# Optimization experiments

Hardware: AMD Instinct MI355X
Metric: run time of the kernel (lower is better)

Reference implementation:

```python
import jax, jax.numpy as jnp
import numpy as np

N = 100000   # nodes
E = 1250000  # directed edges
F = 32       # node_features
H = 64       # hidden_channels
C = 10       # num_classes
NEG_SLOPE = 0.2  # GATConv default LeakyReLU slope


def _glorot(key, shape):
    fan_in = shape[0]
    return jax.random.normal(key, shape, jnp.float32) / np.sqrt(fan_in)


def setup_inputs() -> dict:
    k = jax.random.split(jax.random.key(0), 16)
    x = jax.random.normal(k[0], (N, F), jnp.float32)
    edge_index = jax.random.randint(k[1], (2, E), 0, N, dtype=jnp.int32)
    return {
        "x": x,
        "edge_index": edge_index,
        # GCNConv 1
        "W1": _glorot(k[2], (F, H)), "b1": jnp.zeros((H,), jnp.float32),
        # GATConv (heads=1)
        "W2": _glorot(k[3], (H, H)),
        "a_src": _glorot(k[4], (H,)), "a_dst": _glorot(k[5], (H,)),
        "b2": jnp.zeros((H,), jnp.float32),
        # GCNConv 3
        "W3": _glorot(k[6], (H, H)), "b3": jnp.zeros((H,), jnp.float32),
        # optimization head
        "Wopt": _glorot(k[7], (H, C)), "bopt": jnp.zeros((C,), jnp.float32),
        # bottleneck detector MLP
        "Wb1": _glorot(k[8], (H, 32)), "bb1": jnp.zeros((32,), jnp.float32),
        "Wb2": _glorot(k[9], (32, 1)), "bb2": jnp.zeros((1,), jnp.float32),
    }


def _gcn_conv(x, W, b, src, dst, n):
    # PyG GCNConv: self-loops already appended to src/dst by caller.
    h = x @ W  # [n, out]
    deg = jnp.zeros((n,), x.dtype).at[dst].add(1.0)
    dinv = jax.lax.rsqrt(jnp.maximum(deg, 1e-12))
    norm = dinv[src] * dinv[dst]  # [e]
    msg = h[src] * norm[:, None]  # gather + scale
    out = jnp.zeros_like(h).at[dst].add(msg)  # scatter-add
    return out + b


def _gat_conv(x, W, a_src, a_dst, b, src, dst, n):
    # PyG GATConv, heads=1: self-loops already appended.
    h = x @ W  # [n, out]
    alpha_s = h @ a_src  # [n]
    alpha_d = h @ a_dst  # [n]
    e = jax.nn.leaky_relu(alpha_s[src] + alpha_d[dst], NEG_SLOPE)  # [e]
    # softmax over incoming edges of each dst node
    emax = jax.ops.segment_max(e, dst, num_segments=n)
    p = jnp.exp(e - emax[dst])
    denom = jax.ops.segment_sum(p, dst, num_segments=n)
    alpha = p / denom[dst]
    out = jnp.zeros_like(h).at[dst].add(h[src] * alpha[:, None])
    return out + b


def reference(x, edge_index, W1, b1, W2, a_src, a_dst, b2, W3, b3,
              Wopt, bopt, Wb1, bb1, Wb2, bb2):
    n = x.shape[0]
    loops = jnp.arange(n, dtype=edge_index.dtype)
    src = jnp.concatenate([edge_index[0], loops])
    dst = jnp.concatenate([edge_index[1], loops])

    h = jax.nn.relu(_gcn_conv(x, W1, b1, src, dst, n))
    h = jax.nn.relu(_gat_conv(h, W2, a_src, a_dst, b2, src, dst, n))
    h = jax.nn.relu(_gcn_conv(h, W3, b3, src, dst, n))

    optimizations = h @ Wopt + bopt                     # [n, C]
    bottlenecks = jax.nn.sigmoid(jax.nn.relu(h @ Wb1 + bb1) @ Wb2 + bb2)  # [n, 1]
    graph_embedding = h.mean(axis=0)                    # [H]
    return optimizations, bottlenecks, graph_embedding
```

## Files before the change

### kernel.cpp

```cpp
#include <hip/hip_runtime.h>
#include <hip/hip_bf16.h>


#define CAP 64

__device__ __forceinline__ int uwave(){
  return __builtin_amdgcn_readfirstlane(threadIdx.x >> 6);
}
__device__ __forceinline__ unsigned short f2bf(float f){
  unsigned u = __float_as_uint(f);
  return (unsigned short)((u + 0x7fffu + ((u >> 16) & 1u)) >> 16);
}
__device__ __forceinline__ float bfl(unsigned u){ return __uint_as_float(u << 16); }
__device__ __forceinline__ float bfh(unsigned u){ return __uint_as_float(u & 0xffff0000u); }

__global__ void k_setup(const float* __restrict__ Wopt, const float* __restrict__ bopt,
                        const float* __restrict__ Wb1, const float* __restrict__ bb1,
                        float* __restrict__ Wcat, float* __restrict__ bcat,
                        int* __restrict__ cnt, unsigned short* __restrict__ tb,
                        unsigned short* __restrict__ xh, float* __restrict__ emb_acc,
                        int n){
  int i = blockIdx.x*blockDim.x + threadIdx.x;
  if (i < n) cnt[i] = 0;
  if (blockIdx.x == 0){
    int tid = threadIdx.x;
    for (int j = tid; j < 4096; j += 256){
      int f = j >> 6, c = j & 63;
      float w = 0.f;
      if (c < 10)       w = Wopt[f*10 + c];
      else if (c >= 32) w = Wb1[f*32 + (c-32)];
      Wcat[j] = w;
    }
    if (tid < 64){
      float b = 0.f;
      if (tid < 10)       b = bopt[tid];
      else if (tid >= 32) b = bb1[tid-32];
      bcat[tid] = b;
      tb[(size_t)n*64 + tid] = 0;
      emb_acc[tid] = 0.f;
    }
    if (tid >= 64 && tid < 96) xh[(size_t)n*32 + (tid-64)] = 0;
  }
}

__global__ void k_hist(const int* __restrict__ src, const int* __restrict__ dst,
                       int* __restrict__ cnt, int* __restrict__ adj,
                       int e, int nper){
  int slice = blockIdx.x & 7;
  int i = (blockIdx.x >> 3)*blockDim.x + threadIdx.x;
  if (i >= e) return;
  int d = __builtin_nontemporal_load(&dst[i]);
  int lo = slice*nper;
  if (d < lo || d >= lo + nper) return;
  int pos = atomicAdd(&cnt[d], 1);
  if (pos < CAP){
    int sv = __builtin_nontemporal_load(&src[i]);
    adj[(size_t)d*CAP + pos] = sv;
  }
}

__global__ void k_castscale(const float* __restrict__ x, const int* __restrict__ cnt,
                            unsigned short* __restrict__ xh, int total4){
  int i = blockIdx.x*blockDim.x + threadIdx.x;
  if (i >= total4) return;
  int row = i >> 3;
  float dv = rsqrtf((float)(cnt[row] + 1));
  float4 v = ((const float4*)x)[i];
  uint2 o;
  o.x = (unsigned)f2bf(v.x*dv) | ((unsigned)f2bf(v.y*dv) << 16);
  o.y = (unsigned)f2bf(v.z*dv) | ((unsigned)f2bf(v.w*dv) << 16);
  ((uint2*)xh)[i] = o;
}

__global__ __launch_bounds__(256) void k_agg32g(const unsigned short* __restrict__ xh,
                          const int* __restrict__ adj, const int* __restrict__ cnt,
                          const float* __restrict__ W1, const float* __restrict__ b1,
                          float* __restrict__ h, int n){
  int lane = threadIdx.x & 63;
  float wreg[32];
  #pragma unroll
  for (int k = 0; k < 32; k++) wreg[k] = W1[k*64 + lane];
  float br = b1[lane];
  int v0 = blockIdx.x*8 + uwave()*2;
  if (v0 >= n) return;
  int v1 = v0 + 1;
  bool has1 = v1 < n;
  if (!has1) v1 = v0;
  int cn0 = cnt[v0], cn1 = cnt[v1];
  int c0 = min(cn0, CAP), c1 = min(cn1, CAP);
  int ureg0 = n, ureg1 = n;
  if (lane < c0) ureg0 = (adj + (size_t)v0*CAP)[lane];
  if (lane < c1) ureg1 = (adj + (size_t)v1*CAP)[lane];
  int g = lane >> 3, q = lane & 7;
  float4 a0 = {0.f,0.f,0.f,0.f}, a1 = {0.f,0.f,0.f,0.f};
  int itm = (max(c0, c1) + 7) >> 3;
  #pragma unroll 2
  for (int jj = 0; jj < itm; jj++){
    int u0 = __shfl(ureg0, jj*8 + g);
    int u1 = __shfl(ureg1, jj*8 + g);
    uint2 r0 = ((const uint2*)(xh + (size_t)u0*32))[q];
    uint2 r1 = ((const uint2*)(xh + (size_t)u1*32))[q];
    a0.x += bfl(r0.x); a0.y += bfh(r0.x); a0.z += bfl(r0.y); a0.w += bfh(r0.y);
    a1.x += bfl(r1.x); a1.y += bfh(r1.x); a1.z += bfl(r1.y); a1.w += bfh(r1.y);
  }
  #pragma unroll
  for (int off = 8; off <= 32; off <<= 1){
    a0.x += __shfl_xor(a0.x, off); a0.y += __shfl_xor(a0.y, off);
    a0.z += __shfl_xor(a0.z, off); a0.w += __shfl_xor(a0.w, off);
    a1.x += __shfl_xor(a1.x, off); a1.y += __shfl_xor(a1.y, off);
    a1.z += __shfl_xor(a1.z, off); a1.w += __shfl_xor(a1.w, off);
  }
  uint2 s0 = ((const uint2*)(xh + (size_t)v0*32))[q];
  uint2 s1 = ((const uint2*)(xh + (size_t)v1*32))[q];
  a0.x += bfl(s0.x); a0.y += bfh(s0.x); a0.z += bfl(s0.y); a0.w += bfh(s0.y);
  a1.x += bfl(s1.x); a1.y += bfh(s1.x); a1.z += bfl(s1.y); a1.w += bfh(s1.y);
  float dv0 = rsqrtf((float)(cn0 + 1)), dv1 = rsqrtf((float)(cn1 + 1));
  a0.x *= dv0; a0.y *= dv0; a0.z *= dv0; a0.w *= dv0;
  a1.x *= dv1; a1.y *= dv1; a1.z *= dv1; a1.w *= dv1;
  float h0 = br, h1 = br;
  #pragma unroll
  for (int q2 = 0; q2 < 8; q2++){
    float4 w0, w1;
    w0.x = __shfl(a0.x, q2); w0.y = __shfl(a0.y, q2);
    w0.z = __shfl(a0.z, q2); w0.w = __shfl(a0.w, q2);
    w1.x = __shfl(a1.x, q2); w1.y = __shfl(a1.y, q2);
    w1.z = __shfl(a1.z, q2); w1.w = __shfl(a1.w, q2);
    h0 = fmaf(w0.x, wreg[q2*4+0], h0); h1 = fmaf(w1.x, wreg[q2*4+0], h1);
    h0 = fmaf(w0.y, wreg[q2*4+1], h0); h1 = fmaf(w1.y, wreg[q2*4+1], h1);
    h0 = fmaf(w0.z, wreg[q2*4+2], h0); h1 = fmaf(w1.z, wreg[q2*4+2], h1);
    h0 = fmaf(w0.w, wreg[q2*4+3], h0); h1 = fmaf(w1.w, wreg[q2*4+3], h1);
  }
  h[(size_t)v0*64 + lane] = fmaxf(h0, 0.f);
  if (has1) h[(size_t)v1*64 + lane] = fmaxf(h1, 0.f);
}

template<bool SCALE>
__global__ __launch_bounds__(256, 4) void k_gemm_b(const float* __restrict__ x,
                       const float* __restrict__ W, const int* __restrict__ cnt,
                       unsigned short* __restrict__ t, int n){
  int lane = threadIdx.x & 63;
  int gw = blockIdx.x*4 + uwave();
  int nw = gridDim.x*4;
  float wreg[64];
  #pragma unroll
  for (int k = 0; k < 64; k++) wreg[k] = W[k*64 + lane];
  for (int v = gw; v < n; v += nw){
    const float4* xr = (const float4*)(x + (size_t)v*64);
    float acc = 0.f;
    #pragma unroll
    for (int k4 = 0; k4 < 16; k4++){
      float4 xv = xr[k4];
      acc = fmaf(xv.x, wreg[k4*4+0], acc);
      acc = fmaf(xv.y, wreg[k4*4+1], acc);
      acc = fmaf(xv.z, wreg[k4*4+2], acc);
      acc = fmaf(xv.w, wreg[k4*4+3], acc);
    }
    if (SCALE) acc *= rsqrtf((float)(cnt[v] + 1));
    t[(size_t)v*64 + lane] = f2bf(acc);
  }
}

__global__ __launch_bounds__(256, 4) void k_gemm_alpha(const float* __restrict__ x,
                       const float* __restrict__ W,
                       const float* __restrict__ asrc, const float* __restrict__ adst,
                       unsigned short* __restrict__ t, float* __restrict__ als,
                       float* __restrict__ ald, int n){
  int lane = threadIdx.x & 63;
  int gw = blockIdx.x*4 + uwave();
  int nw = gridDim.x*4;
  float wreg[64];
  #pragma unroll
  for (int k = 0; k < 64; k++) wreg[k] = W[k*64 + lane];
  float asr = asrc[lane], adr = adst[lane];
  for (int v = gw; v < n; v += nw){
    const float4* xr = (const float4*)(x + (size_t)v*64);
    float acc = 0.f;
    #pragma unroll
    for (int k4 = 0; k4 < 16; k4++){
      float4 xv = xr[k4];
      acc = fmaf(xv.x, wreg[k4*4+0], acc);
      acc = fmaf(xv.y, wreg[k4*4+1], acc);
      acc = fmaf(xv.z, wreg[k4*4+2], acc);
      acc = fmaf(xv.w, wreg[k4*4+3], acc);
    }
    t[(size_t)v*64 + lane] = f2bf(acc);
    float s1 = acc * asr, s2 = acc * adr;
    #pragma unroll
    for (int off = 32; off; off >>= 1){
      s1 += __shfl_xor(s1, off);
      s2 += __shfl_xor(s2, off);
    }
    if (lane == 0){ als[v] = s1; ald[v] = s2; }
  }
}

__global__ __launch_bounds__(256) void k_gcn_agg(const unsigned short* __restrict__ t,
                          const int* __restrict__ adj, const int* __restrict__ cnt,
                          const float* __restrict__ b, float* __restrict__ h, int n){
  int lane = threadIdx.x & 63;
  int v0 = blockIdx.x*8 + uwave()*2;
  if (v0 >= n) return;
  int v1 = v0 + 1;
  bool has1 = v1 < n;
  if (!has1) v1 = v0;
  int cn0 = cnt[v0], cn1 = cnt[v1];
  int c0 = min(cn0, CAP), c1 = min(cn1, CAP);
  int ureg0 = n, ureg1 = n;
  if (lane < c0) ureg0 = (adj + (size_t)v0*CAP)[lane];
  if (lane < c1) ureg1 = (adj + (size_t)v1*CAP)[lane];
  int g = lane >> 3, q = lane & 7;
  float a0[8] = {0,0,0,0,0,0,0,0}, a1[8] = {0,0,0,0,0,0,0,0};
  int itm = (max(c0, c1) + 7) >> 3;
  #pragma unroll 2
  for (int jj = 0; jj < itm; jj++){
    int u0 = __shfl(ureg0, jj*8 + g);
    int u1 = __shfl(ureg1, jj*8 + g);
    uint4 r0 = ((const uint4*)(t + (size_t)u0*64))[q];
    uint4 r1 = ((const uint4*)(t + (size_t)u1*64))[q];
    a0[0] += bfl(r0.x); a0[1] += bfh(r0.x); a0[2] += bfl(r0.y); a0[3] += bfh(r0.y);
    a0[4] += bfl(r0.z); a0[5] += bfh(r0.z); a0[6] += bfl(r0.w); a0[7] += bfh(r0.w);
    a1[0] += bfl(r1.x); a1[1] += bfh(r1.x); a1[2] += bfl(r1.y); a1[3] += bfh(r1.y);
    a1[4] += bfl(r1.z); a1[5] += bfh(r1.z); a1[6] += bfl(r1.w); a1[7] += bfh(r1.w);
  }
  #pragma unroll
  for (int off = 8; off <= 32; off <<= 1){
    #pragma unroll
    for (int k = 0; k < 8; k++){
      a0[k] += __shfl_xor(a0[k], off);
      a1[k] += __shfl_xor(a1[k], off);
    }
  }
  uint4 s0 = ((const uint4*)(t + (size_t)v0*64))[q];
  uint4 s1 = ((const uint4*)(t + (size_t)v1*64))[q];
  a0[0] += bfl(s0.x); a0[1] += bfh(s0.x); a0[2] += bfl(s0.y); a0[3] += bfh(s0.y);
  a0[4] += bfl(s0.z); a0[5] += bfh(s0.z); a0[6] += bfl(s0.w); a0[7] += bfh(s0.w);
  a1[0] += bfl(s1.x); a1[1] += bfh(s1.x); a1[2] += bfl(s1.y); a1[3] += bfh(s1.y);
  a1[4] += bfl(s1.z); a1[5] += bfh(s1.z); a1[6] += bfl(s1.w); a1[7] += bfh(s1.w);
  float dv0 = rsqrtf((float)(cn0 + 1)), dv1 = rsqrtf((float)(cn1 + 1));
  float4 b0 = ((const float4*)b)[2*q], b1v = ((const float4*)b)[2*q+1];
  if (g == 0){
    float4 r0, r1;
    r0.x = fmaxf(fmaf(a0[0], dv0, b0.x), 0.f);  r0.y = fmaxf(fmaf(a0[1], dv0, b0.y), 0.f);
    r0.z = fmaxf(fmaf(a0[2], dv0, b0.z), 0.f);  r0.w = fmaxf(fmaf(a0[3], dv0, b0.w), 0.f);
    r1.x = fmaxf(fmaf(a0[4], dv0, b1v.x), 0.f); r1.y = fmaxf(fmaf(a0[5], dv0, b1v.y), 0.f);
    r1.z = fmaxf(fmaf(a0[6], dv0, b1v.z), 0.f); r1.w = fmaxf(fmaf(a0[7], dv0, b1v.w), 0.f);
    ((float4*)(h + (size_t)v0*64))[2*q]   = r0;
    ((float4*)(h + (size_t)v0*64))[2*q+1] = r1;
  } else if (g == 1 && has1){
    float4 r0, r1;
    r0.x = fmaxf(fmaf(a1[0], dv1, b0.x), 0.f);  r0.y = fmaxf(fmaf(a1[1], dv1, b0.y), 0.f);
    r0.z = fmaxf(fmaf(a1[2], dv1, b0.z), 0.f);  r0.w = fmaxf(fmaf(a1[3], dv1, b0.w), 0.f);
    r1.x = fmaxf(fmaf(a1[4], dv1, b1v.x), 0.f); r1.y = fmaxf(fmaf(a1[5], dv1, b1v.y), 0.f);
    r1.z = fmaxf(fmaf(a1[6], dv1, b1v.z), 0.f); r1.w = fmaxf(fmaf(a1[7], dv1, b1v.w), 0.f);
    ((float4*)(h + (size_t)v1*64))[2*q]   = r0;
    ((float4*)(h + (size_t)v1*64))[2*q+1] = r1;
  }
}

__global__ __launch_bounds__(256) void k_gat_agg(const unsigned short* __restrict__ t,
                          const int* __restrict__ adj, const int* __restrict__ cnt,
                          const float* __restrict__ als, const float* __restrict__ ald,
                          const float* __restrict__ b, float* __restrict__ h, int n){
  int lane = threadIdx.x & 63;
  int v0 = blockIdx.x*8 + uwave()*2;
  if (v0 >= n) return;
  int v1 = v0 + 1;
  bool has1 = v1 < n;
  if (!has1) v1 = v0;
  int c0 = min(cnt[v0], CAP), c1 = min(cnt[v1], CAP);
  int ureg0 = n, ureg1 = n;
  if (lane < c0) ureg0 = (adj + (size_t)v0*CAP)[lane];
  if (lane < c1) ureg1 = (adj + (size_t)v1*CAP)[lane];
  int us0 = (lane < c0) ? ureg0 : v0;
  int us1 = (lane < c1) ? ureg1 : v1;
  float adv0 = ald[v0], adv1 = ald[v1];
  float e0 = als[us0] + adv0;
  float e1 = als[us1] + adv1;
  e0 = e0 > 0.f ? e0 : 0.2f*e0;
  e1 = e1 > 0.f ? e1 : 0.2f*e1;
  float es0 = als[v0] + adv0; es0 = es0 > 0.f ? es0 : 0.2f*es0;
  float es1 = als[v1] + adv1; es1 = es1 > 0.f ? es1 : 0.2f*es1;
  float em0 = (lane < c0) ? e0 : -1e30f;
  float em1 = (lane < c1) ? e1 : -1e30f;
  #pragma unroll
  for (int off = 32; off; off >>= 1){
    em0 = fmaxf(em0, __shfl_xor(em0, off));
    em1 = fmaxf(em1, __shfl_xor(em1, off));
  }
  em0 = fmaxf(em0, es0); em1 = fmaxf(em1, es1);
  float p0 = (lane < c0) ? __expf(e0 - em0) : 0.f;
  float p1 = (lane < c1) ? __expf(e1 - em1) : 0.f;
  float sm0 = p0, sm1 = p1;
  #pragma unroll
  for (int off = 32; off; off >>= 1){
    sm0 += __shfl_xor(sm0, off);
    sm1 += __shfl_xor(sm1, off);
  }
  float ps0 = __expf(es0 - em0), ps1 = __expf(es1 - em1);
  float inv0 = 1.f / (sm0 + ps0), inv1 = 1.f / (sm1 + ps1);
  int g = lane >> 3, q = lane & 7;
  float a0[8] = {0,0,0,0,0,0,0,0}, a1[8] = {0,0,0,0,0,0,0,0};
  int itm = (max(c0, c1) + 7) >> 3;
  #pragma unroll 2
  for (int jj = 0; jj < itm; jj++){
    int   u0 = __shfl(ureg0, jj*8 + g);
    int   u1 = __shfl(ureg1, jj*8 + g);
    float w0 = __shfl(p0,    jj*8 + g);
    float w1 = __shfl(p1,    jj*8 + g);
    uint4 r0 = ((const uint4*)(t + (size_t)u0*64))[q];
    uint4 r1 = ((const uint4*)(t + (size_t)u1*64))[q];
    a0[0] = fmaf(w0, bfl(r0.x), a0[0]); a0[1] = fmaf(w0, bfh(r0.x), a0[1]);
    a0[2] = fmaf(w0, bfl(r0.y), a0[2]); a0[3] = fmaf(w0, bfh(r0.y), a0[3]);
    a0[4] = fmaf(w0, bfl(r0.z), a0[4]); a0[5] = fmaf(w0, bfh(r0.z), a0[5]);
    a0[6] = fmaf(w0, bfl(r0.w), a0[6]); a0[7] = fmaf(w0, bfh(r0.w), a0[7]);
    a1[0] = fmaf(w1, bfl(r1.x), a1[0]); a1[1] = fmaf(w1, bfh(r1.x), a1[1]);
    a1[2] = fmaf(w1, bfl(r1.y), a1[2]); a1[3] = fmaf(w1, bfh(r1.y), a1[3]);
    a1[4] = fmaf(w1, bfl(r1.z), a1[4]); a1[5] = fmaf(w1, bfh(r1.z), a1[5]);
    a1[6] = fmaf(w1, bfl(r1.w), a1[6]); a1[7] = fmaf(w1, bfh(r1.w), a1[7]);
  }
  #pragma unroll
  for (int off = 8; off <= 32; off <<= 1){
    #pragma unroll
    for (int k = 0; k < 8; k++){
      a0[k] += __shfl_xor(a0[k], off);
      a1[k] += __shfl_xor(a1[k], off);
    }
  }
  uint4 s0 = ((const uint4*)(t + (size_t)v0*64))[q];
  uint4 s1 = ((const uint4*)(t + (size_t)v1*64))[q];
  a0[0] = fmaf(ps0, bfl(s0.x), a0[0]); a0[1] = fmaf(ps0, bfh(s0.x), a0[1]);
  a0[2] = fmaf(ps0, bfl(s0.y), a0[2]); a0[3] = fmaf(ps0, bfh(s0.y), a0[3]);
  a0[4] = fmaf(ps0, bfl(s0.z), a0[4]); a0[5] = fmaf(ps0, bfh(s0.z), a0[5]);
  a0[6] = fmaf(ps0, bfl(s0.w), a0[6]); a0[7] = fmaf(ps0, bfh(s0.w), a0[7]);
  a1[0] = fmaf(ps1, bfl(s1.x), a1[0]); a1[1] = fmaf(ps1, bfh(s1.x), a1[1]);
  a1[2] = fmaf(ps1, bfl(s1.y), a1[2]); a1[3] = fmaf(ps1, bfh(s1.y), a1[3]);
  a1[4] = fmaf(ps1, bfl(s1.z), a1[4]); a1[5] = fmaf(ps1, bfh(s1.z), a1[5]);
  a1[6] = fmaf(ps1, bfl(s1.w), a1[6]); a1[7] = fmaf(ps1, bfh(s1.w), a1[7]);
  float4 b0 = ((const float4*)b)[2*q], b1v = ((const float4*)b)[2*q+1];
  if (g == 0){
    float4 r0, r1;
    r0.x = fmaxf(fmaf(a0[0], inv0, b0.x), 0.f);  r0.y = fmaxf(fmaf(a0[1], inv0, b0.y), 0.f);
    r0.z = fmaxf(fmaf(a0[2], inv0, b0.z), 0.f);  r0.w = fmaxf(fmaf(a0[3], inv0, b0.w), 0.f);
    r1.x = fmaxf(fmaf(a0[4], inv0, b1v.x), 0.f); r1.y = fmaxf(fmaf(a0[5], inv0, b1v.y), 0.f);
    r1.z = fmaxf(fmaf(a0[6], inv0, b1v.z), 0.f); r1.w = fmaxf(fmaf(a0[7], inv0, b1v.w), 0.f);
    ((float4*)(h + (size_t)v0*64))[2*q]   = r0;
    ((float4*)(h + (size_t)v0*64))[2*q+1] = r1;
  } else if (g == 1 && has1){
    float4 r0, r1;
    r0.x = fmaxf(fmaf(a1[0], inv1, b0.x), 0.f);  r0.y = fmaxf(fmaf(a1[1], inv1, b0.y), 0.f);
    r0.z = fmaxf(fmaf(a1[2], inv1, b0.z), 0.f);  r0.w = fmaxf(fmaf(a1[3], inv1, b0.w), 0.f);
    r1.x = fmaxf(fmaf(a1[4], inv1, b1v.x), 0.f); r1.y = fmaxf(fmaf(a1[5], inv1, b1v.y), 0.f);
    r1.z = fmaxf(fmaf(a1[6], inv1, b1v.z), 0.f); r1.w = fmaxf(fmaf(a1[7], inv1, b1v.w), 0.f);
    ((float4*)(h + (size_t)v1*64))[2*q]   = r0;
    ((float4*)(h + (size_t)v1*64))[2*q+1] = r1;
  }
}

__global__ __launch_bounds__(256, 4) void k_heads(const float* __restrict__ h,
                        const float* __restrict__ Wcat, const float* __restrict__ bcat,
                        const float* __restrict__ Wb2, const float* __restrict__ bb2,
                        float* __restrict__ out_opt, float* __restrict__ out_bot, int n){
  int lane = threadIdx.x & 63;
  int gw = blockIdx.x*4 + uwave();
  int nw = gridDim.x*4;
  float wreg[64];
  #pragma unroll
  for (int k = 0; k < 64; k++) wreg[k] = Wcat[k*64 + lane];
  float bcr  = bcat[lane];
  float wb2r = (lane >= 32) ? Wb2[lane-32] : 0.f;
  float bb2r = bb2[0];
  for (int v = gw; v < n; v += nw){
    const float4* xr = (const float4*)(h + (size_t)v*64);
    float acc = bcr;
    #pragma unroll
    for (int k4 = 0; k4 < 16; k4++){
      float4 xv = xr[k4];
      acc = fmaf(xv.x, wreg[k4*4+0], acc);
      acc = fmaf(xv.y, wreg[k4*4+1], acc);
      acc = fmaf(xv.z, wreg[k4*4+2], acc);
      acc = fmaf(xv.w, wreg[k4*4+3], acc);
    }
    if (lane < 10) out_opt[(size_t)v*10 + lane] = acc;
    float contrib = fmaxf(acc, 0.f) * wb2r;
    #pragma unroll
    for (int off = 32; off; off >>= 1) contrib += __shfl_xor(contrib, off);
    if (lane == 0) out_bot[v] = 1.f / (1.f + __expf(-(contrib + bb2r)));
  }
}

__global__ __launch_bounds__(256) void k_mean(const float* __restrict__ h,
                       float* __restrict__ emb_acc, int n){
  __shared__ float red[256];
  int tid = threadIdx.x;
  int w = tid >> 6, lane = tid & 63;
  float s = 0.f;
  for (int r = blockIdx.x*4 + w; r < n; r += 1024)
    s += h[(size_t)r*64 + lane];
  red[tid] = s;
  __syncthreads();
  if (tid < 64)
    atomicAdd(&emb_acc[tid], red[tid] + red[64+tid] + red[128+tid] + red[192+tid]);
}

__global__ void k_embed(const float* __restrict__ emb_acc, float* __restrict__ out_emb,
                        float invn){
  if (threadIdx.x < 64) out_emb[threadIdx.x] = emb_acc[threadIdx.x] * invn;
}

extern "C" void kernel_launch(void* const* d_in, const int* in_sizes, int n_in,
                              void* d_out, int out_size, void* d_ws, size_t ws_size,
                              hipStream_t stream) {
  const float* x    = (const float*)d_in[0];
  const int*   ei   = (const int*)d_in[1];
  const float* W1   = (const float*)d_in[2];
  const float* b1   = (const float*)d_in[3];
  const float* W2   = (const float*)d_in[4];
  const float* a_s  = (const float*)d_in[5];
  const float* a_d  = (const float*)d_in[6];
  const float* b2   = (const float*)d_in[7];
  const float* W3   = (const float*)d_in[8];
  const float* b3   = (const float*)d_in[9];
  const float* Wopt = (const float*)d_in[10];
  const float* bopt = (const float*)d_in[11];
  const float* Wb1  = (const float*)d_in[12];
  const float* bb1  = (const float*)d_in[13];
  const float* Wb2  = (const float*)d_in[14];
  const float* bb2  = (const float*)d_in[15];

  int n = in_sizes[0] / 32;
  int e = in_sizes[1] / 2;
  const int* src = ei;
  const int* dst = ei + e;

  char* ws = (char*)d_ws;
  size_t off = 0;
  auto alloc = [&](size_t bytes) -> void* {
    void* p = ws + off;
    off += (bytes + 255) & ~(size_t)255;
    return p;
  };
  int*            cnt     = (int*)           alloc((size_t)n * 4);
  int*            adj     = (int*)           alloc((size_t)n * CAP * 4);
  float*          als     = (float*)         alloc((size_t)n * 4);
  float*          ald     = (float*)         alloc((size_t)n * 4);
  unsigned short* xh      = (unsigned short*)alloc((size_t)(n+1) * 32 * 2);
  unsigned short* tb      = (unsigned short*)alloc((size_t)(n+1) * 64 * 2);
  float*          hbuf    = (float*)         alloc((size_t)n * 64 * 4);
  float*          emb_acc = (float*)         alloc((size_t)64 * 4);
  float*          Wcat    = (float*)         alloc((size_t)4096 * 4);
  float*          bcat    = (float*)         alloc((size_t)64 * 4);

  float* out_opt = (float*)d_out;
  float* out_bot = out_opt + (size_t)n * 10;
  float* out_emb = out_bot + n;

  int nb8    = (n + 7) / 8;
  int nbN    = (n + 255) / 256;
  int nbE    = (e + 255) / 256;
  int nper   = (n + 7) / 8;
  int total4 = n*32/4;
  int nbC    = (total4 + 255) / 256;

  k_setup<<<nbN, 256, 0, stream>>>(Wopt, bopt, Wb1, bb1, Wcat, bcat,
                                   cnt, tb, xh, emb_acc, n);
  k_hist<<<nbE*8, 256, 0, stream>>>(src, dst, cnt, adj, e, nper);
  k_castscale<<<nbC, 256, 0, stream>>>(x, cnt, xh, total4);

  k_agg32g<<<nb8, 256, 0, stream>>>(xh, adj, cnt, W1, b1, hbuf, n);

  k_gemm_alpha<<<1024, 256, 0, stream>>>(hbuf, W2, a_s, a_d, tb, als, ald, n);
  k_gat_agg<<<nb8, 256, 0, stream>>>(tb, adj, cnt, als, ald, b2, hbuf, n);

  k_gemm_b<true><<<1024, 256, 0, stream>>>(hbuf, W3, cnt, tb, n);
  k_gcn_agg<<<nb8, 256, 0, stream>>>(tb, adj, cnt, b3, hbuf, n);

  k_heads<<<1024, 256, 0, stream>>>(hbuf, Wcat, bcat, Wb2, bb2,
                                    out_opt, out_bot, n);
  k_mean<<<256, 256, 0, stream>>>(hbuf, emb_acc, n);
  k_embed<<<1, 64, 0, stream>>>(emb_acc, out_emb, 1.0f / (float)n);
}
```

Baseline: 426.3 us.

## Store intermediate hidden activations as bf16 and halve histogram slicing

The shared hidden buffer between layers changes from fp32 to bf16. Every producer (aggregation kernels) now packs bf16 and every consumer (GEMMs, heads, mean) unpacks it, which halves activation read/write traffic. The edge histogram pass also drops from 8 destination slices to 4, so the edge list is re-read fewer times at the cost of less locality per pass. The extra rounding of activations to bf16 adds some precision loss.

```diff
diff --git a/kernel.cpp b/kernel.cpp
--- a/kernel.cpp
+++ b/kernel.cpp
@@ -3,6 +3,7 @@
 
 
 #define CAP 64
+#define NSLICE 4
 
 __device__ __forceinline__ int uwave(){
   return __builtin_amdgcn_readfirstlane(threadIdx.x >> 6);
@@ -46,8 +47,8 @@
 __global__ void k_hist(const int* __restrict__ src, const int* __restrict__ dst,
                        int* __restrict__ cnt, int* __restrict__ adj,
                        int e, int nper){
-  int slice = blockIdx.x & 7;
-  int i = (blockIdx.x >> 3)*blockDim.x + threadIdx.x;
+  int slice = blockIdx.x & (NSLICE-1);
+  int i = (blockIdx.x / NSLICE)*blockDim.x + threadIdx.x;
   if (i >= e) return;
   int d = __builtin_nontemporal_load(&dst[i]);
   int lo = slice*nper;
@@ -75,7 +76,7 @@
 __global__ __launch_bounds__(256) void k_agg32g(const unsigned short* __restrict__ xh,
                           const int* __restrict__ adj, const int* __restrict__ cnt,
                           const float* __restrict__ W1, const float* __restrict__ b1,
-                          float* __restrict__ h, int n){
+                          unsigned short* __restrict__ h, int n){
   int lane = threadIdx.x & 63;
   float wreg[32];
   #pragma unroll
@@ -117,7 +118,7 @@
   float dv0 = rsqrtf((float)(cn0 + 1)), dv1 = rsqrtf((float)(cn1 + 1));
   a0.x *= dv0; a0.y *= dv0; a0.z *= dv0; a0.w *= dv0;
   a1.x *= dv1; a1.y *= dv1; a1.z *= dv1; a1.w *= dv1;
-  float h0 = br, h1 = br;
+  float h0 = br, h1v = br;
   #pragma unroll
   for (int q2 = 0; q2 < 8; q2++){
     float4 w0, w1;
@@ -125,17 +126,17 @@
     w0.z = __shfl(a0.z, q2); w0.w = __shfl(a0.w, q2);
     w1.x = __shfl(a1.x, q2); w1.y = __shfl(a1.y, q2);
     w1.z = __shfl(a1.z, q2); w1.w = __shfl(a1.w, q2);
-    h0 = fmaf(w0.x, wreg[q2*4+0], h0); h1 = fmaf(w1.x, wreg[q2*4+0], h1);
-    h0 = fmaf(w0.y, wreg[q2*4+1], h0); h1 = fmaf(w1.y, wreg[q2*4+1], h1);
-    h0 = fmaf(w0.z, wreg[q2*4+2], h0); h1 = fmaf(w1.z, wreg[q2*4+2], h1);
-    h0 = fmaf(w0.w, wreg[q2*4+3], h0); h1 = fmaf(w1.w, wreg[q2*4+3], h1);
-  }
-  h[(size_t)v0*64 + lane] = fmaxf(h0, 0.f);
-  if (has1) h[(size_t)v1*64 + lane] = fmaxf(h1, 0.f);
+    h0 = fmaf(w0.x, wreg[q2*4+0], h0); h1v = fmaf(w1.x, wreg[q2*4+0], h1v);
+    h0 = fmaf(w0.y, wreg[q2*4+1], h0); h1v = fmaf(w1.y, wreg[q2*4+1], h1v);
+    h0 = fmaf(w0.z, wreg[q2*4+2], h0); h1v = fmaf(w1.z, wreg[q2*4+2], h1v);
+    h0 = fmaf(w0.w, wreg[q2*4+3], h0); h1v = fmaf(w1.w, wreg[q2*4+3], h1v);
+  }
+  h[(size_t)v0*64 + lane] = f2bf(fmaxf(h0, 0.f));
+  if (has1) h[(size_t)v1*64 + lane] = f2bf(fmaxf(h1v, 0.f));
 }
 
 template<bool SCALE>
-__global__ __launch_bounds__(256, 4) void k_gemm_b(const float* __restrict__ x,
+__global__ __launch_bounds__(256, 4) void k_gemm_b(const unsigned short* __restrict__ x,
                        const float* __restrict__ W, const int* __restrict__ cnt,
                        unsigned short* __restrict__ t, int n){
   int lane = threadIdx.x & 63;
@@ -145,22 +146,26 @@
   #pragma unroll
   for (int k = 0; k < 64; k++) wreg[k] = W[k*64 + lane];
   for (int v = gw; v < n; v += nw){
-    const float4* xr = (const float4*)(x + (size_t)v*64);
+    const uint4* xr = (const uint4*)(x + (size_t)v*64);
     float acc = 0.f;
     #pragma unroll
-    for (int k4 = 0; k4 < 16; k4++){
-      float4 xv = xr[k4];
-      acc = fmaf(xv.x, wreg[k4*4+0], acc);
-      acc = fmaf(xv.y, wreg[k4*4+1], acc);
-      acc = fmaf(xv.z, wreg[k4*4+2], acc);
-      acc = fmaf(xv.w, wreg[k4*4+3], acc);
+    for (int k8 = 0; k8 < 8; k8++){
+      uint4 c = xr[k8];
+      acc = fmaf(bfl(c.x), wreg[k8*8+0], acc);
+      acc = fmaf(bfh(c.x), wreg[k8*8+1], acc);
+      acc = fmaf(bfl(c.y), wreg[k8*8+2], acc);
+      acc = fmaf(bfh(c.y), wreg[k8*8+3], acc);
+      acc = fmaf(bfl(c.z), wreg[k8*8+4], acc);
+      acc = fmaf(bfh(c.z), wreg[k8*8+5], acc);
+      acc = fmaf(bfl(c.w), wreg[k8*8+6], acc);
+      acc = fmaf(bfh(c.w), wreg[k8*8+7], acc);
     }
     if (SCALE) acc *= rsqrtf((float)(cnt[v] + 1));
     t[(size_t)v*64 + lane] = f2bf(acc);
   }
 }
 
-__global__ __launch_bounds__(256, 4) void k_gemm_alpha(const float* __restrict__ x,
+__global__ __launch_bounds__(256, 4) void k_gemm_alpha(const unsigned short* __restrict__ x,
                        const float* __restrict__ W,
                        const float* __restrict__ asrc, const float* __restrict__ adst,
                        unsigned short* __restrict__ t, float* __restrict__ als,
@@ -173,15 +178,19 @@
   for (int k = 0; k < 64; k++) wreg[k] = W[k*64 + lane];
   float asr = asrc[lane], adr = adst[lane];
   for (int v = gw; v < n; v += nw){
-    const float4* xr = (const float4*)(x + (size_t)v*64);
+    const uint4* xr = (const uint4*)(x + (size_t)v*64);
     float acc = 0.f;
     #pragma unroll
-    for (int k4 = 0; k4 < 16; k4++){
-      float4 xv = xr[k4];
-      acc = fmaf(xv.x, wreg[k4*4+0], acc);
-      acc = fmaf(xv.y, wreg[k4*4+1], acc);
-      acc = fmaf(xv.z, wreg[k4*4+2], acc);
-      acc = fmaf(xv.w, wreg[k4*4+3], acc);
+    for (int k8 = 0; k8 < 8; k8++){
+      uint4 c = xr[k8];
+      acc = fmaf(bfl(c.x), wreg[k8*8+0], acc);
+      acc = fmaf(bfh(c.x), wreg[k8*8+1], acc);
+      acc = fmaf(bfl(c.y), wreg[k8*8+2], acc);
+      acc = fmaf(bfh(c.y), wreg[k8*8+3], acc);
+      acc = fmaf(bfl(c.z), wreg[k8*8+4], acc);
+      acc = fmaf(bfh(c.z), wreg[k8*8+5], acc);
+      acc = fmaf(bfl(c.w), wreg[k8*8+6], acc);
+      acc = fmaf(bfh(c.w), wreg[k8*8+7], acc);
     }
     t[(size_t)v*64 + lane] = f2bf(acc);
     float s1 = acc * asr, s2 = acc * adr;
@@ -196,7 +205,7 @@
 
 __global__ __launch_bounds__(256) void k_gcn_agg(const unsigned short* __restrict__ t,
                           const int* __restrict__ adj, const int* __restrict__ cnt,
-                          const float* __restrict__ b, float* __restrict__ h, int n){
+                          const float* __restrict__ b, unsigned short* __restrict__ h, int n){
   int lane = threadIdx.x & 63;
   int v0 = blockIdx.x*8 + uwave()*2;
   if (v0 >= n) return;
@@ -239,28 +248,34 @@
   float dv0 = rsqrtf((float)(cn0 + 1)), dv1 = rsqrtf((float)(cn1 + 1));
   float4 b0 = ((const float4*)b)[2*q], b1v = ((const float4*)b)[2*q+1];
   if (g == 0){
-    float4 r0, r1;
-    r0.x = fmaxf(fmaf(a0[0], dv0, b0.x), 0.f);  r0.y = fmaxf(fmaf(a0[1], dv0, b0.y), 0.f);
-    r0.z = fmaxf(fmaf(a0[2], dv0, b0.z), 0.f);  r0.w = fmaxf(fmaf(a0[3], dv0, b0.w), 0.f);
-    r1.x = fmaxf(fmaf(a0[4], dv0, b1v.x), 0.f); r1.y = fmaxf(fmaf(a0[5], dv0, b1v.y), 0.f);
-    r1.z = fmaxf(fmaf(a0[6], dv0, b1v.z), 0.f); r1.w = fmaxf(fmaf(a0[7], dv0, b1v.w), 0.f);
-    ((float4*)(h + (size_t)v0*64))[2*q]   = r0;
-    ((float4*)(h + (size_t)v0*64))[2*q+1] = r1;
+    float r0 = fmaxf(fmaf(a0[0], dv0, b0.x), 0.f),  r1 = fmaxf(fmaf(a0[1], dv0, b0.y), 0.f);
+    float r2 = fmaxf(fmaf(a0[2], dv0, b0.z), 0.f),  r3 = fmaxf(fmaf(a0[3], dv0, b0.w), 0.f);
+    float r4 = fmaxf(fmaf(a0[4], dv0, b1v.x), 0.f), r5 = fmaxf(fmaf(a0[5], dv0, b1v.y), 0.f);
+    float r6 = fmaxf(fmaf(a0[6], dv0, b1v.z), 0.f), r7 = fmaxf(fmaf(a0[7], dv0, b1v.w), 0.f);
+    uint4 o;
+    o.x = (unsigned)f2bf(r0) | ((unsigned)f2bf(r1) << 16);
+    o.y = (unsigned)f2bf(r2) | ((unsigned)f2bf(r3) << 16);
+    o.z = (unsigned)f2bf(r4) | ((unsigned)f2bf(r5) << 16);
+    o.w = (unsigned)f2bf(r6) | ((unsigned)f2bf(r7) << 16);
+    ((uint4*)(h + (size_t)v0*64))[q] = o;
   } else if (g == 1 && has1){
-    float4 r0, r1;
-    r0.x = fmaxf(fmaf(a1[0], dv1, b0.x), 0.f);  r0.y = fmaxf(fmaf(a1[1], dv1, b0.y), 0.f);
-    r0.z = fmaxf(fmaf(a1[2], dv1, b0.z), 0.f);  r0.w = fmaxf(fmaf(a1[3], dv1, b0.w), 0.f);
-    r1.x = fmaxf(fmaf(a1[4], dv1, b1v.x), 0.f); r1.y = fmaxf(fmaf(a1[5], dv1, b1v.y), 0.f);
-    r1.z = fmaxf(fmaf(a1[6], dv1, b1v.z), 0.f); r1.w = fmaxf(fmaf(a1[7], dv1, b1v.w), 0.f);
-    ((float4*)(h + (size_t)v1*64))[2*q]   = r0;
-    ((float4*)(h + (size_t)v1*64))[2*q+1] = r1;
+    float r0 = fmaxf(fmaf(a1[0], dv1, b0.x), 0.f),  r1 = fmaxf(fmaf(a1[1], dv1, b0.y), 0.f);
+    float r2 = fmaxf(fmaf(a1[2], dv1, b0.z), 0.f),  r3 = fmaxf(fmaf(a1[3], dv1, b0.w), 0.f);
+    float r4 = fmaxf(fmaf(a1[4], dv1, b1v.x), 0.f), r5 = fmaxf(fmaf(a1[5], dv1, b1v.y), 0.f);
+    float r6 = fmaxf(fmaf(a1[6], dv1, b1v.z), 0.f), r7 = fmaxf(fmaf(a1[7], dv1, b1v.w), 0.f);
+    uint4 o;
+    o.x = (unsigned)f2bf(r0) | ((unsigned)f2bf(r1) << 16);
+    o.y = (unsigned)f2bf(r2) | ((unsigned)f2bf(r3) << 16);
+    o.z = (unsigned)f2bf(r4) | ((unsigned)f2bf(r5) << 16);
+    o.w = (unsigned)f2bf(r6) | ((unsigned)f2bf(r7) << 16);
+    ((uint4*)(h + (size_t)v1*64))[q] = o;
   }
 }
 
 __global__ __launch_bounds__(256) void k_gat_agg(const unsigned short* __restrict__ t,
                           const int* __restrict__ adj, const int* __restrict__ cnt,
                           const float* __restrict__ als, const float* __restrict__ ald,
-                          const float* __restrict__ b, float* __restrict__ h, int n){
+                          const float* __restrict__ b, unsigned short* __restrict__ h, int n){
   int lane = threadIdx.x & 63;
   int v0 = blockIdx.x*8 + uwave()*2;
   if (v0 >= n) return;
@@ -338,25 +353,31 @@
   a1[6] = fmaf(ps1, bfl(s1.w), a1[6]); a1[7] = fmaf(ps1, bfh(s1.w), a1[7]);
   float4 b0 = ((const float4*)b)[2*q], b1v = ((const float4*)b)[2*q+1];
   if (g == 0){
-    float4 r0, r1;
-    r0.x = fmaxf(fmaf(a0[0], inv0, b0.x), 0.f);  r0.y = fmaxf(fmaf(a0[1], inv0, b0.y), 0.f);
-    r0.z = fmaxf(fmaf(a0[2], inv0, b0.z), 0.f);  r0.w = fmaxf(fmaf(a0[3], inv0, b0.w), 0.f);
-    r1.x = fmaxf(fmaf(a0[4], inv0, b1v.x), 0.f); r1.y = fmaxf(fmaf(a0[5], inv0, b1v.y), 0.f);
-    r1.z = fmaxf(fmaf(a0[6], inv0, b1v.z), 0.f); r1.w = fmaxf(fmaf(a0[7], inv0, b1v.w), 0.f);
-    ((float4*)(h + (size_t)v0*64))[2*q]   = r0;
-    ((float4*)(h + (size_t)v0*64))[2*q+1] = r1;
+    float r0 = fmaxf(fmaf(a0[0], inv0, b0.x), 0.f),  r1 = fmaxf(fmaf(a0[1], inv0, b0.y), 0.f);
+    float r2 = fmaxf(fmaf(a0[2], inv0, b0.z), 0.f),  r3 = fmaxf(fmaf(a0[3], inv0, b0.w), 0.f);
+    float r4 = fmaxf(fmaf(a0[4], inv0, b1v.x), 0.f), r5 = fmaxf(fmaf(a0[5], inv0, b1v.y), 0.f);
+    float r6 = fmaxf(fmaf(a0[6], inv0, b1v.z), 0.f), r7 = fmaxf(fmaf(a0[7], inv0, b1v.w), 0.f);
+    uint4 o;
+    o.x = (unsigned)f2bf(r0) | ((unsigned)f2bf(r1) << 16);
+    o.y = (unsigned)f2bf(r2) | ((unsigned)f2bf(r3) << 16);
+    o.z = (unsigned)f2bf(r4) | ((unsigned)f2bf(r5) << 16);
+    o.w = (unsigned)f2bf(r6) | ((unsigned)f2bf(r7) << 16);
+    ((uint4*)(h + (size_t)v0*64))[q] = o;
   } else if (g == 1 && has1){
-    float4 r0, r1;
-    r0.x = fmaxf(fmaf(a1[0], inv1, b0.x), 0.f);  r0.y = fmaxf(fmaf(a1[1], inv1, b0.y), 0.f);
-    r0.z = fmaxf(fmaf(a1[2], inv1, b0.z), 0.f);  r0.w = fmaxf(fmaf(a1[3], inv1, b0.w), 0.f);
-    r1.x = fmaxf(fmaf(a1[4], inv1, b1v.x), 0.f); r1.y = fmaxf(fmaf(a1[5], inv1, b1v.y), 0.f);
-    r1.z = fmaxf(fmaf(a1[6], inv1, b1v.z), 0.f); r1.w = fmaxf(fmaf(a1[7], inv1, b1v.w), 0.f);
-    ((float4*)(h + (size_t)v1*64))[2*q]   = r0;
-    ((float4*)(h + (size_t)v1*64))[2*q+1] = r1;
-  }
-}
-
-__global__ __launch_bounds__(256, 4) void k_heads(const float* __restrict__ h,
+    float r0 = fmaxf(fmaf(a1[0], inv1, b0.x), 0.f),  r1 = fmaxf(fmaf(a1[1], inv1, b0.y), 0.f);
+    float r2 = fmaxf(fmaf(a1[2], inv1, b0.z), 0.f),  r3 = fmaxf(fmaf(a1[3], inv1, b0.w), 0.f);
+    float r4 = fmaxf(fmaf(a1[4], inv1, b1v.x), 0.f), r5 = fmaxf(fmaf(a1[5], inv1, b1v.y), 0.f);
+    float r6 = fmaxf(fmaf(a1[6], inv1, b1v.z), 0.f), r7 = fmaxf(fmaf(a1[7], inv1, b1v.w), 0.f);
+    uint4 o;
+    o.x = (unsigned)f2bf(r0) | ((unsigned)f2bf(r1) << 16);
+    o.y = (unsigned)f2bf(r2) | ((unsigned)f2bf(r3) << 16);
+    o.z = (unsigned)f2bf(r4) | ((unsigned)f2bf(r5) << 16);
+    o.w = (unsigned)f2bf(r6) | ((unsigned)f2bf(r7) << 16);
+    ((uint4*)(h + (size_t)v1*64))[q] = o;
+  }
+}
+
+__global__ __launch_bounds__(256, 4) void k_heads(const unsigned short* __restrict__ h,
                         const float* __restrict__ Wcat, const float* __restrict__ bcat,
                         const float* __restrict__ Wb2, const float* __restrict__ bb2,
                         float* __restrict__ out_opt, float* __restrict__ out_bot, int n){
@@ -370,15 +391,19 @@
   float wb2r = (lane >= 32) ? Wb2[lane-32] : 0.f;
   float bb2r = bb2[0];
   for (int v = gw; v < n; v += nw){
-    const float4* xr = (const float4*)(h + (size_t)v*64);
+    const uint4* xr = (const uint4*)(h + (size_t)v*64);
     float acc = bcr;
     #pragma unroll
-    for (int k4 = 0; k4 < 16; k4++){
-      float4 xv = xr[k4];
-      acc = fmaf(xv.x, wreg[k4*4+0], acc);
-      acc = fmaf(xv.y, wreg[k4*4+1], acc);
-      acc = fmaf(xv.z, wreg[k4*4+2], acc);
-      acc = fmaf(xv.w, wreg[k4*4+3], acc);
+    for (int k8 = 0; k8 < 8; k8++){
+      uint4 c = xr[k8];
+      acc = fmaf(bfl(c.x), wreg[k8*8+0], acc);
+      acc = fmaf(bfh(c.x), wreg[k8*8+1], acc);
+      acc = fmaf(bfl(c.y), wreg[k8*8+2], acc);
+      acc = fmaf(bfh(c.y), wreg[k8*8+3], acc);
+      acc = fmaf(bfl(c.z), wreg[k8*8+4], acc);
+      acc = fmaf(bfh(c.z), wreg[k8*8+5], acc);
+      acc = fmaf(bfl(c.w), wreg[k8*8+6], acc);
+      acc = fmaf(bfh(c.w), wreg[k8*8+7], acc);
     }
     if (lane < 10) out_opt[(size_t)v*10 + lane] = acc;
     float contrib = fmaxf(acc, 0.f) * wb2r;
@@ -388,14 +413,14 @@
   }
 }
 
-__global__ __launch_bounds__(256) void k_mean(const float* __restrict__ h,
+__global__ __launch_bounds__(256) void k_mean(const unsigned short* __restrict__ h,
                        float* __restrict__ emb_acc, int n){
   __shared__ float red[256];
   int tid = threadIdx.x;
   int w = tid >> 6, lane = tid & 63;
   float s = 0.f;
   for (int r = blockIdx.x*4 + w; r < n; r += 1024)
-    s += h[(size_t)r*64 + lane];
+    s += __uint_as_float(((unsigned)h[(size_t)r*64 + lane]) << 16);
   red[tid] = s;
   __syncthreads();
   if (tid < 64)
@@ -445,7 +470,7 @@
   float*          ald     = (float*)         alloc((size_t)n * 4);
   unsigned short* xh      = (unsigned short*)alloc((size_t)(n+1) * 32 * 2);
   unsigned short* tb      = (unsigned short*)alloc((size_t)(n+1) * 64 * 2);
-  float*          hbuf    = (float*)         alloc((size_t)n * 64 * 4);
+  unsigned short* hbuf    = (unsigned short*)alloc((size_t)n * 64 * 2);
   float*          emb_acc = (float*)         alloc((size_t)64 * 4);
   float*          Wcat    = (float*)         alloc((size_t)4096 * 4);
   float*          bcat    = (float*)         alloc((size_t)64 * 4);
@@ -457,13 +482,13 @@
   int nb8    = (n + 7) / 8;
   int nbN    = (n + 255) / 256;
   int nbE    = (e + 255) / 256;
-  int nper   = (n + 7) / 8;
+  int nper   = (n + NSLICE - 1) / NSLICE;
   int total4 = n*32/4;
   int nbC    = (total4 + 255) / 256;
 
   k_setup<<<nbN, 256, 0, stream>>>(Wopt, bopt, Wb1, bb1, Wcat, bcat,
                                    cnt, tb, xh, emb_acc, n);
-  k_hist<<<nbE*8, 256, 0, stream>>>(src, dst, cnt, adj, e, nper);
+  k_hist<<<nbE*NSLICE, 256, 0, stream>>>(src, dst, cnt, adj, e, nper);
   k_castscale<<<nbC, 256, 0, stream>>>(x, cnt, xh, total4);
 
   k_agg32g<<<nb8, 256, 0, stream>>>(xh, adj, cnt, W1, b1, hbuf, n);
```

Measured after the change: 399.6 us. -6.3%, faster.
